# Kernel optimization log

Hardware: AMD Instinct MI355X
Metric: run time of the kernel (lower is better)

## Reference

```python
import jax, jax.numpy as jnp
import numpy as np

BS, NA, NT, ED, AD, NC = 64, 900, 600, 256, 11, 10
CONF_DECAY = 0.6


def _topk_gather(conf, k, *xs):
    # conf: [bs, N] -> top-k values + gather rows of each x: [bs, N, d] -> [bs, k, d]
    vals, idx = jax.lax.top_k(conf, k)
    outs = [jnp.take_along_axis(x, idx[:, :, None], axis=1) for x in xs]
    return vals, outs


def setup_inputs() -> dict:
    key = jax.random.key(0)
    ks = jax.random.split(key, 7)
    return {
        "instance_feature": jax.random.normal(ks[0], (BS, NA, ED), jnp.float32),
        "anchor": jax.random.normal(ks[1], (BS, NA, AD), jnp.float32),
        "confidence": jax.random.normal(ks[2], (BS, NA, NC), jnp.float32),
        "cached_feature": jax.random.normal(ks[3], (BS, NT, ED), jnp.float32),
        "cached_anchor": jax.random.normal(ks[4], (BS, NT, AD), jnp.float32),
        "prev_confidence": jax.random.uniform(ks[5], (BS, NT), jnp.float32),
        "mask": jax.random.bernoulli(ks[6], 0.8, (BS,)),
    }


def reference(instance_feature, anchor, confidence, cached_feature, cached_anchor, prev_confidence, mask):
    # ---- InstanceBank.update ----
    N = NA - NT  # number of fresh instances kept alongside the temporal cache
    conf_max = confidence.max(axis=-1)  # [bs, NA]
    _, (sel_f, sel_a) = _topk_gather(conf_max, N, instance_feature, anchor)
    sel_f = jnp.concatenate([cached_feature, sel_f], axis=1)  # [bs, NA, ED]
    sel_a = jnp.concatenate([cached_anchor, sel_a], axis=1)   # [bs, NA, AD]
    m = mask[:, None, None]
    feat = jnp.where(m, sel_f, instance_feature)
    anc = jnp.where(m, sel_a, anchor)

    # ---- InstanceBank.cache (detached path) ----
    conf_c = jax.nn.sigmoid(jax.lax.stop_gradient(conf_max))
    conf_c = conf_c.at[:, :NT].set(jnp.maximum(prev_confidence * CONF_DECAY, conf_c[:, :NT]))
    new_conf, (cf, ca) = _topk_gather(
        conf_c, NT, jax.lax.stop_gradient(feat), jax.lax.stop_gradient(anc)
    )

    merged = jnp.concatenate([feat, anc], axis=-1)  # [bs, NA, ED+AD]
    return merged, new_conf, cf, ca
```

## Files before the change

### kernel.cpp

```cpp
#include <hip/hip_runtime.h>

#define BS   64
#define NA   900
#define NT   600
#define NSEL 300
#define ED   256
#define AD   11
#define NC   10
#define SORTN 1024
#define CACHED_FLAG 0x40000000

#define OFF_MERGED  0
#define OFF_NEWCONF (BS * NA * (ED + AD))
#define OFF_CF      (OFF_NEWCONF + BS * NT)
#define OFF_CA      (OFF_CF + BS * NT * ED)

__device__ __forceinline__ unsigned int fkey(float x) {
    unsigned int u = __float_as_uint(x);
    return (u & 0x80000000u) ? ~u : (u | 0x80000000u);
}

__device__ __forceinline__ unsigned long long shfl_xor64(unsigned long long v, int m) {
    return (unsigned long long)__shfl_xor((long long)v, m, 64);
}

__device__ __forceinline__ void sort1024(unsigned long long& key, int i,
                                         unsigned long long* lds) {
    for (int k = 2; k <= SORTN; k <<= 1) {
        for (int j = k >> 1; j > 0; j >>= 1) {
            unsigned long long partner;
            if (j >= 64) {
                __syncthreads();
                lds[i] = key;
                __syncthreads();
                partner = lds[i ^ j];
            } else {
                partner = shfl_xor64(key, j);
            }
            const bool up      = ((i & k) == 0);
            const bool lower   = ((i & j) == 0);
            const bool keepmin = (lower == up);
            const bool pgt     = (key > partner);
            key = (keepmin == pgt) ? partner : key;
        }
    }
}

__global__ __launch_bounds__(1024) void topk_kernel(
    const float* __restrict__ confidence,
    const float* __restrict__ prev_conf,
    const int*   __restrict__ mask,
    float*       __restrict__ new_conf_out,
    int*         __restrict__ src_map,
    int*         __restrict__ idx2_out)
{
    __shared__ unsigned long long keys[SORTN];
    __shared__ float cc_s[NA];

    const int b = blockIdx.x;
    const int i = threadIdx.x;

    float cmax = 0.0f;
    if (i < NA) {
        const float* cp = confidence + ((size_t)b * NA + i) * NC;
        float m = cp[0];
        #pragma unroll
        for (int k = 1; k < NC; k++) m = fmaxf(m, cp[k]);
        cmax = m;
    }

    unsigned long long key = (i < NA)
        ? ((((unsigned long long)(~fkey(cmax))) << 32) | (unsigned int)i)
        : 0xFFFFFFFFFFFFFFFFull;
    sort1024(key, i, keys);

    __syncthreads();
    int* rank = (int*)keys;
    rank[i] = (int)(key & 0xFFFFFFFFull);
    __syncthreads();

    const int mk = mask[b];
    if (i < NA) {
        int s;
        if (mk) {
            s = (i < NT) ? (i | CACHED_FLAG) : rank[i - NT];
        } else {
            s = i;
        }
        src_map[(size_t)b * NA + i] = s;
    }

    float c = 0.0f;
    if (i < NA) {
        double d = 1.0 / (1.0 + exp(-(double)cmax));
        c = (float)d;
        if (i < NT) c = fmaxf(prev_conf[(size_t)b * NT + i] * 0.6f, c);
        cc_s[i] = c;
    }
    __syncthreads();

    key = (i < NA)
        ? ((((unsigned long long)(~fkey(c))) << 32) | (unsigned int)i)
        : 0xFFFFFFFFFFFFFFFFull;
    sort1024(key, i, keys);

    if (i < NT) {
        int r = (int)(key & 0xFFFFFFFFull);
        idx2_out[(size_t)b * NT + i]     = r;
        new_conf_out[(size_t)b * NT + i] = cc_s[r];
    }
}

__global__ __launch_bounds__(256) void gather_kernel(
    const float* __restrict__ inst_f,
    const float* __restrict__ anchor,
    const float* __restrict__ cached_f,
    const float* __restrict__ cached_a,
    const int*   __restrict__ src_map,
    const int*   __restrict__ idx2,
    float*       __restrict__ out)
{
    const int wave = threadIdx.x >> 6;
    const int lane = threadIdx.x & 63;
    const int gr   = blockIdx.x * 4 + wave;
    if (gr >= BS * (NA + NT)) return;

    const int b = gr / (NA + NT);
    const int t = gr - b * (NA + NT);

    int row = (t < NA) ? t : idx2[(size_t)b * NT + (t - NA)];
    const int s = src_map[(size_t)b * NA + row];

    const float* fsrc;
    const float* asrc;
    if (s & CACHED_FLAG) {
        const int r = s & 0xFFFF;
        fsrc = cached_f + ((size_t)b * NT + r) * ED;
        asrc = cached_a + ((size_t)b * NT + r) * AD;
    } else {
        fsrc = inst_f + ((size_t)b * NA + s) * ED;
        asrc = anchor + ((size_t)b * NA + s) * AD;
    }

    if (t < NA) {
        float* orow = out + OFF_MERGED + ((size_t)b * NA + t) * (ED + AD);
        const float4 v = ((const float4*)fsrc)[lane];
        orow[4 * lane + 0] = v.x;
        orow[4 * lane + 1] = v.y;
        orow[4 * lane + 2] = v.z;
        orow[4 * lane + 3] = v.w;
        if (lane < AD) orow[ED + lane] = asrc[lane];
    } else {
        const int j = t - NA;
        float4*       crow = (float4*)(out + OFF_CF + ((size_t)b * NT + j) * ED);
        const float4* f4   = (const float4*)fsrc;
        crow[lane] = f4[lane];
        if (lane < AD) out[OFF_CA + ((size_t)b * NT + j) * AD + lane] = asrc[lane];
    }
}

extern "C" void kernel_launch(void* const* d_in, const int* in_sizes, int n_in,
                              void* d_out, int out_size, void* d_ws, size_t ws_size,
                              hipStream_t stream) {
    const float* inst_f = (const float*)d_in[0];
    const float* anchor = (const float*)d_in[1];
    const float* conf   = (const float*)d_in[2];
    const float* cach_f = (const float*)d_in[3];
    const float* cach_a = (const float*)d_in[4];
    const float* prevc  = (const float*)d_in[5];
    const int*   mask   = (const int*)d_in[6];
    float* out = (float*)d_out;

    int* src_map = (int*)d_ws;
    int* idx2    = src_map + BS * NA;

    topk_kernel<<<BS, 1024, 0, stream>>>(conf, prevc, mask,
                                         out + OFF_NEWCONF, src_map, idx2);

    const int nrows = BS * (NA + NT);
    gather_kernel<<<(nrows + 3) / 4, 256, 0, stream>>>(
        inst_f, anchor, cach_f, cach_a, src_map, idx2, out);
}
```

Baseline: 213.1 us.

## Scatter cache rows from merged gather via inverse top-k positions

The top-k kernel now writes an inverse map (row -> cache slot or -1) instead of the forward cache index list. The gather kernel then walks only the 900 merged rows per batch, reads each source row once, and scatters it to both the merged output and, when selected, its cache slot. This removes the second read of 600 feature rows per batch and the extra wave launches, at the cost of scattered writes to the cache outputs and an extra index load per row.

```diff
diff --git a/kernel.cpp b/kernel.cpp
--- a/kernel.cpp
+++ b/kernel.cpp
@@ -52,7 +52,7 @@
     const int*   __restrict__ mask,
     float*       __restrict__ new_conf_out,
     int*         __restrict__ src_map,
-    int*         __restrict__ idx2_out)
+    int*         __restrict__ pos2)
 {
     __shared__ unsigned long long keys[SORTN];
     __shared__ float cc_s[NA];
@@ -106,8 +106,11 @@
 
     if (i < NT) {
         int r = (int)(key & 0xFFFFFFFFull);
-        idx2_out[(size_t)b * NT + i]     = r;
         new_conf_out[(size_t)b * NT + i] = cc_s[r];
+        pos2[(size_t)b * NA + r] = i;
+    } else if (i < NA) {
+        int r = (int)(key & 0xFFFFFFFFull);
+        pos2[(size_t)b * NA + r] = -1;
     }
 }
 
@@ -117,19 +120,19 @@
     const float* __restrict__ cached_f,
     const float* __restrict__ cached_a,
     const int*   __restrict__ src_map,
-    const int*   __restrict__ idx2,
+    const int*   __restrict__ pos2,
     float*       __restrict__ out)
 {
     const int wave = threadIdx.x >> 6;
     const int lane = threadIdx.x & 63;
     const int gr   = blockIdx.x * 4 + wave;
-    if (gr >= BS * (NA + NT)) return;
+    if (gr >= BS * NA) return;
 
-    const int b = gr / (NA + NT);
-    const int t = gr - b * (NA + NT);
+    const int b = gr / NA;
+    const int t = gr - b * NA;
 
-    int row = (t < NA) ? t : idx2[(size_t)b * NT + (t - NA)];
-    const int s = src_map[(size_t)b * NA + row];
+    const int s = src_map[(size_t)b * NA + t];
+    const int p = pos2[(size_t)b * NA + t];
 
     const float* fsrc;
     const float* asrc;
@@ -142,20 +145,21 @@
         asrc = anchor + ((size_t)b * NA + s) * AD;
     }
 
-    if (t < NA) {
-        float* orow = out + OFF_MERGED + ((size_t)b * NA + t) * (ED + AD);
-        const float4 v = ((const float4*)fsrc)[lane];
-        orow[4 * lane + 0] = v.x;
-        orow[4 * lane + 1] = v.y;
-        orow[4 * lane + 2] = v.z;
-        orow[4 * lane + 3] = v.w;
-        if (lane < AD) orow[ED + lane] = asrc[lane];
-    } else {
-        const int j = t - NA;
-        float4*       crow = (float4*)(out + OFF_CF + ((size_t)b * NT + j) * ED);
-        const float4* f4   = (const float4*)fsrc;
-        crow[lane] = f4[lane];
-        if (lane < AD) out[OFF_CA + ((size_t)b * NT + j) * AD + lane] = asrc[lane];
+    const float4 v = ((const float4*)fsrc)[lane];
+    float av = 0.0f;
+    if (lane < AD) av = asrc[lane];
+
+    float* orow = out + OFF_MERGED + ((size_t)b * NA + t) * (ED + AD);
+    orow[4 * lane + 0] = v.x;
+    orow[4 * lane + 1] = v.y;
+    orow[4 * lane + 2] = v.z;
+    orow[4 * lane + 3] = v.w;
+    if (lane < AD) orow[ED + lane] = av;
+
+    if (p >= 0) {
+        float4* crow = (float4*)(out + OFF_CF + ((size_t)b * NT + p) * ED);
+        crow[lane] = v;
+        if (lane < AD) out[OFF_CA + ((size_t)b * NT + p) * AD + lane] = av;
     }
 }
 
@@ -172,12 +176,12 @@
     float* out = (float*)d_out;
 
     int* src_map = (int*)d_ws;
-    int* idx2    = src_map + BS * NA;
+    int* pos2    = src_map + BS * NA;
 
     topk_kernel<<<BS, 1024, 0, stream>>>(conf, prevc, mask,
-                                         out + OFF_NEWCONF, src_map, idx2);
+                                         out + OFF_NEWCONF, src_map, pos2);
 
-    const int nrows = BS * (NA + NT);
+    const int nrows = BS * NA;
     gather_kernel<<<(nrows + 3) / 4, 256, 0, stream>>>(
-        inst_f, anchor, cach_f, cach_a, src_map, idx2, out);
+        inst_f, anchor, cach_f, cach_a, src_map, pos2, out);
 }
```

Result: no change. 209.3 us (-1.8%).
